# Kernel optimization log

Measured on AMD Instinct MI355X. Metric: run time of the kernel, lower is better.

Reference implementation:

```python
import jax, jax.numpy as jnp
import numpy as np

N = 50000          # total points (25 clouds x 2000 pts)
C = 64             # feature channels (in == out, no bottleneck)
K_NN = 16          # neighbors kept per dilation branch
DILATIONS = (1, 2, 4)
KMAX = K_NN * max(DILATIONS)   # base kNN graph has k*d_max neighbors per node
B = 25             # number of point clouds
EPS = 1e-16


def setup_inputs() -> dict:
    key = jax.random.key(0)
    ks = jax.random.split(key, 8)
    x = jax.random.normal(ks[0], (N, C), jnp.float32)
    pos = jax.random.normal(ks[1], (N, 3), jnp.float32)
    # kNN-style edge_index [2, N*KMAX]: row0 = source/neighbor j, row1 = center i,
    # KMAX consecutive edges per center node, neighbors restricted to the same cloud.
    pts = N // B
    cloud_base = (jnp.arange(N) // pts) * pts
    src = cloud_base[:, None] + jax.random.randint(ks[2], (N, KMAX), 0, pts)
    dst = jnp.broadcast_to(jnp.arange(N)[:, None], (N, KMAX))
    edge_index = jnp.stack([src.reshape(-1), dst.reshape(-1)]).astype(jnp.int32)
    batch = jnp.repeat(jnp.arange(B), pts).astype(jnp.int32)
    nD = len(DILATIONS)
    s = 1.0 / np.sqrt(C)
    Wv = jax.random.normal(ks[3], (nD, C, C), jnp.float32) * s   # lin (value)
    Wq = jax.random.normal(ks[4], (nD, C, C), jnp.float32) * s   # lin_dst
    Wk = jax.random.normal(ks[5], (nD, C, C), jnp.float32) * s   # lin_src
    Wp = jax.random.normal(ks[6], (nD, 3, C), jnp.float32) * (1.0 / np.sqrt(3.0))  # pos_nn
    bp = jax.random.normal(ks[7], (nD, C), jnp.float32) * 0.01
    return dict(x=x, pos=pos, Wv=Wv, Wq=Wq, Wk=Wk, Wp=Wp, bp=bp,
                edge_index=edge_index, batch=batch)


def _dilated_edges(edge_index, k, d):
    # take every d-th of the first k*d neighbors within each node's block -> k edges/node
    e = edge_index.reshape(2, -1, KMAX)[:, :, : k * d : d]
    return e.reshape(2, -1)


def _segment_softmax(a, seg, n):
    amax = jax.ops.segment_max(a, seg, num_segments=n)
    e = jnp.exp(a - amax[seg])
    s = jax.ops.segment_sum(e, seg, num_segments=n)
    return e / (s[seg] + EPS)


def _pt_conv(x, pos, src, dst, Wv, Wq, Wk, Wp, bp):
    # PyG PointTransformerConv: msg = softmax_i(q_i - k_j + delta_ij) * (v_j + delta_ij)
    n = x.shape[0]
    q = x @ Wq        # [N, C]  (lin_dst)
    kk = x @ Wk       # [N, C]  (lin_src)
    v = x @ Wv        # [N, C]  (lin, value)
    delta = (pos[dst] - pos[src]) @ Wp + bp            # [E, C] positional encoding
    alpha = _segment_softmax(q[dst] - kk[src] + delta, dst, n)
    return jax.ops.segment_sum(alpha * (v[src] + delta), dst, num_segments=n)


def reference(x, pos, Wv, Wq, Wk, Wp, bp, edge_index, batch):
    inputs = x
    res = None
    for i, d in enumerate(DILATIONS):
        e = _dilated_edges(edge_index, K_NN, d)
        h = _pt_conv(x, pos, e[0], e[1], Wv[i], Wq[i], Wk[i], Wp[i], bp[i])
        res = h if res is None else jnp.maximum(res, h)   # stack+max over branches
    # global max pool per cloud, gathered back per node
    pool = jax.ops.segment_max(x, batch, num_segments=B)[batch]
    res = jnp.maximum(res, pool)
    return res + inputs   # residual
```

## Files before the change

kernel.cpp:

```cpp
#include <hip/hip_runtime.h>
#include <math.h>

#define NP 50000
#define CH 64
#define KMAX 64
#define KNN 16
#define NB 25
#define PTS (NP / NB)
#define EPSF 1e-16f
#define NTILES (NP / 16)
#define ATILES (NP / 4)
#define L2E 1.4426950408889634f
#define LN2 0.6931471805599453f

typedef __attribute__((ext_vector_type(8))) short short8;
typedef __attribute__((ext_vector_type(4))) float float4v;
typedef __attribute__((ext_vector_type(4))) unsigned int uint4v;
typedef __attribute__((ext_vector_type(2))) unsigned int uint2v;
typedef __attribute__((ext_vector_type(4))) unsigned short ushort4v;

__device__ __forceinline__ ushort f2b(float f) {
  unsigned u = __float_as_uint(f);
  unsigned r = (u + 0x7FFFu + ((u >> 16) & 1u)) >> 16;
  return (ushort)r;
}
__device__ __forceinline__ float b2f(ushort h) {
  return __uint_as_float(((unsigned)h) << 16);
}

#define QBF_BYTES   ((size_t)3 * NP * CH * 2)
#define KVP_BYTES   ((size_t)3 * NP * CH * 4)
#define XBF_BYTES   ((size_t)NP * CH * 2)
#define WPACK_ELEMS (9 * 4 * 2 * 64 * 8)
#define XV (NP * CH / 4)

__global__ __launch_bounds__(256) void prep_kernel(
    const float* __restrict__ x,
    const float* __restrict__ Wv,
    const float* __restrict__ Wq,
    const float* __restrict__ Wk,
    ushort* __restrict__ x_bf,
    ushort* __restrict__ wpack,
    float* __restrict__ pool) {
  const int tid = threadIdx.x;
  const int bid = blockIdx.x;
  __shared__ float red[4][CH];

  if (bid < NB) {
    const int lane = tid & 63;
    const int wave = tid >> 6;
    const float* xb = x + (size_t)bid * PTS * CH;
    float m0 = -INFINITY, m1 = -INFINITY, m2 = -INFINITY, m3 = -INFINITY;
    for (int r = wave * 4; r < PTS; r += 16) {
      m0 = fmaxf(m0, xb[(size_t)(r + 0) * CH + lane]);
      m1 = fmaxf(m1, xb[(size_t)(r + 1) * CH + lane]);
      m2 = fmaxf(m2, xb[(size_t)(r + 2) * CH + lane]);
      m3 = fmaxf(m3, xb[(size_t)(r + 3) * CH + lane]);
    }
    red[wave][lane] = fmaxf(fmaxf(m0, m1), fmaxf(m2, m3));
    __syncthreads();
    if (wave == 0) {
      pool[bid * CH + lane] = fmaxf(fmaxf(red[0][lane], red[1][lane]),
                                    fmaxf(red[2][lane], red[3][lane]));
    }
  } else {
    const int gid = (bid - NB) * 256 + tid;
    if (gid < XV) {
      const float4* xv = (const float4*)x;
      float4 v = xv[gid];
      ushort4v o;
      o[0] = f2b(v.x); o[1] = f2b(v.y); o[2] = f2b(v.z); o[3] = f2b(v.w);
      *(ushort4v*)(x_bf + (size_t)gid * 4) = o;
    } else {
      int pid = gid - XV;
      if (pid < WPACK_ELEMS) {
        int j     = pid & 7;
        int lane  = (pid >> 3) & 63;
        int kstep = (pid >> 9) & 1;
        int mtile = (pid >> 10) & 3;
        int mat   = pid >> 12;
        const float* W;
        int d;
        float scale;
        if (mat < 3)      { W = Wq; d = mat;     scale = L2E; }
        else if (mat < 6) { W = Wk; d = mat - 3; scale = L2E; }
        else              { W = Wv; d = mat - 6; scale = 1.f; }
        int oc = mtile * 16 + (lane & 15);
        int ic = kstep * 32 + ((lane >> 4) & 3) * 8 + j;
        wpack[pid] = f2b(W[d * CH * CH + ic * CH + oc] * scale);
      }
    }
  }
}

__global__ __launch_bounds__(256) void qkv_mfma(
    const ushort* __restrict__ x_bf,
    const ushort* __restrict__ wpack,
    ushort* __restrict__ qbf,
    unsigned int* __restrict__ kvp) {
  const int lane = threadIdx.x;
  const int tile = blockIdx.x * 4 + threadIdx.y;
  if (tile >= NTILES) return;
  const int y = blockIdx.y;
  const int kbase = (lane >> 4) * 8;
  const int myNode = tile * 16 + (lane & 15);
  const ushort* xr = x_bf + (size_t)myNode * CH;
  short8 b0 = *(const short8*)(xr + kbase);
  short8 b1 = *(const short8*)(xr + 32 + kbase);

  if (y < 3) {
    const int dd = y;
    ushort* outQ = qbf + (size_t)dd * NP * CH;
#pragma unroll
    for (int mt = 0; mt < 4; ++mt) {
      short8 a0 = *(const short8*)(wpack +
          ((((size_t)dd * 4 + mt) * 2 + 0) * 64 + lane) * 8);
      short8 a1 = *(const short8*)(wpack +
          ((((size_t)dd * 4 + mt) * 2 + 1) * 64 + lane) * 8);
      float4v acc = {0.f, 0.f, 0.f, 0.f};
      acc = __builtin_amdgcn_mfma_f32_16x16x32_bf16(a0, b0, acc, 0, 0, 0);
      acc = __builtin_amdgcn_mfma_f32_16x16x32_bf16(a1, b1, acc, 0, 0, 0);
      int oc = mt * 16 + (lane >> 4) * 4;
      uint2v o;
      o[0] = (unsigned)f2b(acc[0]) | ((unsigned)f2b(acc[1]) << 16);
      o[1] = (unsigned)f2b(acc[2]) | ((unsigned)f2b(acc[3]) << 16);
      *(uint2v*)(outQ + (size_t)myNode * CH + oc) = o;
    }
  } else {
    const int dd = y - 3;
    unsigned int* outKV = kvp + (size_t)dd * NP * CH;
#pragma unroll
    for (int mt = 0; mt < 4; ++mt) {
      short8 k0 = *(const short8*)(wpack +
          ((((size_t)(3 + dd) * 4 + mt) * 2 + 0) * 64 + lane) * 8);
      short8 k1 = *(const short8*)(wpack +
          ((((size_t)(3 + dd) * 4 + mt) * 2 + 1) * 64 + lane) * 8);
      short8 v0 = *(const short8*)(wpack +
          ((((size_t)(6 + dd) * 4 + mt) * 2 + 0) * 64 + lane) * 8);
      short8 v1 = *(const short8*)(wpack +
          ((((size_t)(6 + dd) * 4 + mt) * 2 + 1) * 64 + lane) * 8);
      float4v aK = {0.f, 0.f, 0.f, 0.f};
      float4v aV = {0.f, 0.f, 0.f, 0.f};
      aK = __builtin_amdgcn_mfma_f32_16x16x32_bf16(k0, b0, aK, 0, 0, 0);
      aK = __builtin_amdgcn_mfma_f32_16x16x32_bf16(k1, b1, aK, 0, 0, 0);
      aV = __builtin_amdgcn_mfma_f32_16x16x32_bf16(v0, b0, aV, 0, 0, 0);
      aV = __builtin_amdgcn_mfma_f32_16x16x32_bf16(v1, b1, aV, 0, 0, 0);
      int oc = mt * 16 + (lane >> 4) * 4;
      uint4v o;
#pragma unroll
      for (int i = 0; i < 4; ++i)
        o[i] = ((unsigned)f2b(aK[i]) << 16) | (unsigned)f2b(aV[i]);
      *(uint4v*)(outKV + (size_t)myNode * CH + oc) = o;
    }
  }
}

__global__ __launch_bounds__(384, 6) void attn_kernel(
    const float* __restrict__ x,
    const float* __restrict__ pos,
    const float* __restrict__ Wp,
    const float* __restrict__ bp,
    const int*   __restrict__ edge_src,
    const ushort* __restrict__ qbf,
    const unsigned int* __restrict__ kvp,
    const float* __restrict__ pool,
    float* __restrict__ out) {
  const int bx  = blockIdx.x;
  const int xcd = bx & 7;
  const int kk  = bx >> 3;
  const int base = (ATILES * xcd) >> 3;
  const int cnt  = ((ATILES * (xcd + 1)) >> 3) - base;
  if (kk >= cnt) return;
  const int node0 = (base + kk) * 4;

  const int wy   = threadIdx.y;
  const int dd   = wy % 3;
  const int half = wy / 3;
  const int tid  = wy * 64 + threadIdx.x;

  __shared__ float sEdge[4 * 260];
  __shared__ float sPartS[3 * 4 * 68];
  __shared__ float sPartA[3 * 4 * 68];
  __shared__ float sRes[2 * 4 * 68];

  if (tid < 256) {
    int nl = tid >> 6, p = tid & 63;
    int nd = node0 + nl;
    int j = edge_src[(size_t)nd * KMAX + p];
    float4v w;
    w[0] = pos[nd * 3 + 0] - pos[j * 3 + 0];
    w[1] = pos[nd * 3 + 1] - pos[j * 3 + 1];
    w[2] = pos[nd * 3 + 2] - pos[j * 3 + 2];
    w[3] = __int_as_float(j << 8);
    *(float4v*)&sEdge[nl * 260 + p * 4] = w;
  }
  __syncthreads();

  const int lane = threadIdx.x;
  const int g    = lane >> 4;
  const int cl   = lane & 15;
  const int node = node0 + g;
  const float* sMy = &sEdge[g * 260];
  const unsigned clOfs = (unsigned)(cl << 4);

  float4v bq, wp0, wp1, wp2;
  {
    ushort4v qh = *(const ushort4v*)(qbf + ((size_t)dd * NP + node) * CH + cl * 4);
    const float* WpD = Wp + dd * 192;
    wp0 = *(const float4v*)(WpD + 0 * 64 + cl * 4) * L2E;
    wp1 = *(const float4v*)(WpD + 1 * 64 + cl * 4) * L2E;
    wp2 = *(const float4v*)(WpD + 2 * 64 + cl * 4) * L2E;
    float4v bpv = *(const float4v*)(bp + dd * 64 + cl * 4);
#pragma unroll
    for (int i = 0; i < 4; ++i) bq[i] = b2f(qh[i]) + bpv[i] * L2E;
  }
  const char* KVb = (const char*)(kvp + (size_t)dd * NP * CH);

  float4v s    = {0.f, 0.f, 0.f, 0.f};
  float4v accv = {0.f, 0.f, 0.f, 0.f};
#pragma unroll
  for (int e = 0; e < 8; ++e) {
    const int p = (half * 8 + e) << dd;
    float4v w = *(const float4v*)(sMy + p * 4);
    uint4v u = *(const uint4v*)(KVb + (__float_as_uint(w[3]) + clOfs));
    float4v kf, vf, wgt;
#pragma unroll
    for (int i = 0; i < 4; ++i) kf[i] = __uint_as_float(u[i] & 0xFFFF0000u);
#pragma unroll
    for (int i = 0; i < 4; ++i) vf[i] = __uint_as_float(u[i] << 16);
    float4v t = bq + w[0] * wp0 + w[1] * wp1 + w[2] * wp2;
    float4v a = t - kf;
#pragma unroll
    for (int i = 0; i < 4; ++i) wgt[i] = __builtin_amdgcn_exp2f(a[i]);
    s += wgt;
    float4v vt;
#pragma unroll
    for (int i = 0; i < 4; ++i) vt[i] = fmaf(LN2, t[i], vf[i]);
    accv += wgt * vt;
  }

  if (half == 1) {
    *(float4v*)&sPartS[(dd * 4 + g) * 68 + cl * 4] = s;
    *(float4v*)&sPartA[(dd * 4 + g) * 68 + cl * 4] = accv;
  }
  __syncthreads();

  float4v r;
  if (half == 0) {
    float4v s2 = *(const float4v*)&sPartS[(dd * 4 + g) * 68 + cl * 4];
    float4v a2 = *(const float4v*)&sPartA[(dd * 4 + g) * 68 + cl * 4];
    s += s2;
    accv += a2;
    float4v bpv = *(const float4v*)(bp + dd * 64 + cl * 4);
#pragma unroll
    for (int i = 0; i < 4; ++i) {
      float q = (bq[i] - bpv[i] * L2E) * LN2;
      r[i] = accv[i] * __builtin_amdgcn_rcpf(s[i] + EPSF) - q;
    }
    if (dd > 0)
      *(float4v*)&sRes[((dd - 1) * 4 + g) * 68 + cl * 4] = r;
  }
  __syncthreads();

  if (wy == 0) {
    float4v r1 = *(const float4v*)&sRes[(0 * 4 + g) * 68 + cl * 4];
    float4v r2 = *(const float4v*)&sRes[(1 * 4 + g) * 68 + cl * 4];
    const int b = node / PTS;
    float4v pv = *(const float4v*)(pool + b * CH + cl * 4);
    float4v xv = *(const float4v*)(x + (size_t)node * CH + cl * 4);
    float4v res;
#pragma unroll
    for (int i = 0; i < 4; ++i)
      res[i] = fmaxf(fmaxf(fmaxf(r[i], r1[i]), r2[i]), pv[i]) + xv[i];
    *(float4v*)(out + (size_t)node * CH + cl * 4) = res;
  }
}

extern "C" void kernel_launch(void* const* d_in, const int* in_sizes, int n_in,
                              void* d_out, int out_size, void* d_ws, size_t ws_size,
                              hipStream_t stream) {
  const float* x    = (const float*)d_in[0];
  const float* pos  = (const float*)d_in[1];
  const float* Wv   = (const float*)d_in[2];
  const float* Wq   = (const float*)d_in[3];
  const float* Wk   = (const float*)d_in[4];
  const float* Wp   = (const float*)d_in[5];
  const float* bp   = (const float*)d_in[6];
  const int*   ei   = (const int*)d_in[7];
  float* out = (float*)d_out;

  char* wsb = (char*)d_ws;
  ushort* qbf   = (ushort*)wsb;
  unsigned int* kvp = (unsigned int*)(wsb + QBF_BYTES);
  ushort* x_bf  = (ushort*)(wsb + QBF_BYTES + KVP_BYTES);
  ushort* wpack = (ushort*)(wsb + QBF_BYTES + KVP_BYTES + XBF_BYTES);
  float*  pool  = (float*)(wsb + QBF_BYTES + KVP_BYTES + XBF_BYTES +
                           (size_t)WPACK_ELEMS * 2);

  {
    int convBlocks = (XV + WPACK_ELEMS + 255) / 256;
    dim3 grid(NB + convBlocks);
    hipLaunchKernelGGL(prep_kernel, grid, dim3(256), 0, stream,
                       x, Wv, Wq, Wk, x_bf, wpack, pool);
  }
  {
    dim3 grid((NTILES + 3) / 4, 6);
    dim3 block(64, 4);
    hipLaunchKernelGGL(qkv_mfma, grid, block, 0, stream, x_bf, wpack, qbf, kvp);
  }
  {
    dim3 grid(8 * ((ATILES + 7) / 8));
    dim3 block(64, 6);
    hipLaunchKernelGGL(attn_kernel, grid, block, 0, stream,
                       x, pos, Wp, bp, ei, qbf, kvp, pool, out);
  }
}
```

Baseline: 218.2 us.

## Split per-cloud max pool across blocks and merge attention halves in one sync

The global max pool now runs over 8 partial blocks per cloud instead of one, so the 25 long-running pool blocks no longer set the tail of the prep kernel. The attention kernel subtracts q*s per half before reduction, so both halves write partial sums and wave 0 does the combine, divide and branch max, removing one __syncthreads and a shared-memory round trip. Consumers now read and reduce 8 partial pool rows per node.

New measurement: 186.7 us. 1.17x faster.

```diff
diff --git a/kernel.cpp b/kernel.cpp
--- a/kernel.cpp
+++ b/kernel.cpp
@@ -12,6 +12,8 @@
 #define ATILES (NP / 4)
 #define L2E 1.4426950408889634f
 #define LN2 0.6931471805599453f
+#define PPB 8
+#define PROWS (PTS / PPB)
 
 typedef __attribute__((ext_vector_type(8))) short short8;
 typedef __attribute__((ext_vector_type(4))) float float4v;
@@ -41,30 +43,30 @@
     const float* __restrict__ Wk,
     ushort* __restrict__ x_bf,
     ushort* __restrict__ wpack,
-    float* __restrict__ pool) {
+    float* __restrict__ poolP) {
   const int tid = threadIdx.x;
   const int bid = blockIdx.x;
   __shared__ float red[4][CH];
 
-  if (bid < NB) {
+  if (bid < NB * PPB) {
     const int lane = tid & 63;
     const int wave = tid >> 6;
-    const float* xb = x + (size_t)bid * PTS * CH;
-    float m0 = -INFINITY, m1 = -INFINITY, m2 = -INFINITY, m3 = -INFINITY;
-    for (int r = wave * 4; r < PTS; r += 16) {
+    const int cloud = bid >> 3;
+    const int part  = bid & 7;
+    const float* xb = x + ((size_t)cloud * PTS + part * PROWS) * CH;
+    float m0 = -INFINITY, m1 = -INFINITY;
+    for (int r = wave * 2; r < PROWS; r += 8) {
       m0 = fmaxf(m0, xb[(size_t)(r + 0) * CH + lane]);
       m1 = fmaxf(m1, xb[(size_t)(r + 1) * CH + lane]);
-      m2 = fmaxf(m2, xb[(size_t)(r + 2) * CH + lane]);
-      m3 = fmaxf(m3, xb[(size_t)(r + 3) * CH + lane]);
-    }
-    red[wave][lane] = fmaxf(fmaxf(m0, m1), fmaxf(m2, m3));
+    }
+    red[wave][lane] = fmaxf(m0, m1);
     __syncthreads();
     if (wave == 0) {
-      pool[bid * CH + lane] = fmaxf(fmaxf(red[0][lane], red[1][lane]),
-                                    fmaxf(red[2][lane], red[3][lane]));
+      poolP[(size_t)bid * CH + lane] = fmaxf(fmaxf(red[0][lane], red[1][lane]),
+                                             fmaxf(red[2][lane], red[3][lane]));
     }
   } else {
-    const int gid = (bid - NB) * 256 + tid;
+    const int gid = (bid - NB * PPB) * 256 + tid;
     if (gid < XV) {
       const float4* xv = (const float4*)x;
       float4 v = xv[gid];
@@ -163,7 +165,7 @@
     const int*   __restrict__ edge_src,
     const ushort* __restrict__ qbf,
     const unsigned int* __restrict__ kvp,
-    const float* __restrict__ pool,
+    const float* __restrict__ poolP,
     float* __restrict__ out) {
   const int bx  = blockIdx.x;
   const int xcd = bx & 7;
@@ -179,9 +181,8 @@
   const int tid  = wy * 64 + threadIdx.x;
 
   __shared__ float sEdge[4 * 260];
-  __shared__ float sPartS[3 * 4 * 68];
-  __shared__ float sPartA[3 * 4 * 68];
-  __shared__ float sRes[2 * 4 * 68];
+  __shared__ float sS[6 * 4 * 68];
+  __shared__ float sP[6 * 4 * 68];
 
   if (tid < 256) {
     int nl = tid >> 6, p = tid & 63;
@@ -200,10 +201,9 @@
   const int g    = lane >> 4;
   const int cl   = lane & 15;
   const int node = node0 + g;
-  const float* sMy = &sEdge[g * 260];
   const unsigned clOfs = (unsigned)(cl << 4);
 
-  float4v bq, wp0, wp1, wp2;
+  float4v bq, qorig, wp0, wp1, wp2;
   {
     ushort4v qh = *(const ushort4v*)(qbf + ((size_t)dd * NP + node) * CH + cl * 4);
     const float* WpD = Wp + dd * 192;
@@ -211,17 +211,23 @@
     wp1 = *(const float4v*)(WpD + 1 * 64 + cl * 4) * L2E;
     wp2 = *(const float4v*)(WpD + 2 * 64 + cl * 4) * L2E;
     float4v bpv = *(const float4v*)(bp + dd * 64 + cl * 4);
-#pragma unroll
-    for (int i = 0; i < 4; ++i) bq[i] = b2f(qh[i]) + bpv[i] * L2E;
+    float4v qf;
+#pragma unroll
+    for (int i = 0; i < 4; ++i) qf[i] = b2f(qh[i]);
+    bq = qf + bpv * L2E;
+    qorig = qf * LN2;
   }
   const char* KVb = (const char*)(kvp + (size_t)dd * NP * CH);
+
+  const float* ep = &sEdge[g * 260] + (((half * 8) << dd) * 4);
+  const int estep = (1 << dd) * 4;
 
   float4v s    = {0.f, 0.f, 0.f, 0.f};
   float4v accv = {0.f, 0.f, 0.f, 0.f};
 #pragma unroll
   for (int e = 0; e < 8; ++e) {
-    const int p = (half * 8 + e) << dd;
-    float4v w = *(const float4v*)(sMy + p * 4);
+    float4v w = *(const float4v*)ep;
+    ep += estep;
     uint4v u = *(const uint4v*)(KVb + (__float_as_uint(w[3]) + clOfs));
     float4v kf, vf, wgt;
 #pragma unroll
@@ -233,45 +239,46 @@
 #pragma unroll
     for (int i = 0; i < 4; ++i) wgt[i] = __builtin_amdgcn_exp2f(a[i]);
     s += wgt;
-    float4v vt;
-#pragma unroll
-    for (int i = 0; i < 4; ++i) vt[i] = fmaf(LN2, t[i], vf[i]);
-    accv += wgt * vt;
-  }
-
-  if (half == 1) {
-    *(float4v*)&sPartS[(dd * 4 + g) * 68 + cl * 4] = s;
-    *(float4v*)&sPartA[(dd * 4 + g) * 68 + cl * 4] = accv;
-  }
+    accv += wgt * (vf + t * LN2);
+  }
+
+  float4v P = accv - qorig * s;
+  *(float4v*)&sS[(wy * 4 + g) * 68 + cl * 4] = s;
+  *(float4v*)&sP[(wy * 4 + g) * 68 + cl * 4] = P;
   __syncthreads();
 
-  float4v r;
-  if (half == 0) {
-    float4v s2 = *(const float4v*)&sPartS[(dd * 4 + g) * 68 + cl * 4];
-    float4v a2 = *(const float4v*)&sPartA[(dd * 4 + g) * 68 + cl * 4];
-    s += s2;
-    accv += a2;
-    float4v bpv = *(const float4v*)(bp + dd * 64 + cl * 4);
-#pragma unroll
-    for (int i = 0; i < 4; ++i) {
-      float q = (bq[i] - bpv[i] * L2E) * LN2;
-      r[i] = accv[i] * __builtin_amdgcn_rcpf(s[i] + EPSF) - q;
-    }
-    if (dd > 0)
-      *(float4v*)&sRes[((dd - 1) * 4 + g) * 68 + cl * 4] = r;
-  }
-  __syncthreads();
-
   if (wy == 0) {
-    float4v r1 = *(const float4v*)&sRes[(0 * 4 + g) * 68 + cl * 4];
-    float4v r2 = *(const float4v*)&sRes[(1 * 4 + g) * 68 + cl * 4];
+    float4v res;
+#pragma unroll
+    for (int d2 = 0; d2 < 3; ++d2) {
+      float4v s0 = *(const float4v*)&sS[((d2    ) * 4 + g) * 68 + cl * 4];
+      float4v s1 = *(const float4v*)&sS[((d2 + 3) * 4 + g) * 68 + cl * 4];
+      float4v p0 = *(const float4v*)&sP[((d2    ) * 4 + g) * 68 + cl * 4];
+      float4v p1 = *(const float4v*)&sP[((d2 + 3) * 4 + g) * 68 + cl * 4];
+      float4v st = s0 + s1;
+      float4v pt = p0 + p1;
+      float4v r;
+#pragma unroll
+      for (int i = 0; i < 4; ++i)
+        r[i] = pt[i] * __builtin_amdgcn_rcpf(st[i] + EPSF);
+      if (d2 == 0) res = r;
+      else {
+#pragma unroll
+        for (int i = 0; i < 4; ++i) res[i] = fmaxf(res[i], r[i]);
+      }
+    }
     const int b = node / PTS;
-    float4v pv = *(const float4v*)(pool + b * CH + cl * 4);
+    const float* pp = poolP + (size_t)(b * PPB) * CH + cl * 4;
+    float4v pv = *(const float4v*)pp;
+#pragma unroll
+    for (int q2 = 1; q2 < PPB; ++q2) {
+      float4v t2 = *(const float4v*)(pp + (size_t)q2 * CH);
+#pragma unroll
+      for (int i = 0; i < 4; ++i) pv[i] = fmaxf(pv[i], t2[i]);
+    }
     float4v xv = *(const float4v*)(x + (size_t)node * CH + cl * 4);
-    float4v res;
-#pragma unroll
-    for (int i = 0; i < 4; ++i)
-      res[i] = fmaxf(fmaxf(fmaxf(r[i], r1[i]), r2[i]), pv[i]) + xv[i];
+#pragma unroll
+    for (int i = 0; i < 4; ++i) res[i] = fmaxf(res[i], pv[i]) + xv[i];
     *(float4v*)(out + (size_t)node * CH + cl * 4) = res;
   }
 }
@@ -294,14 +301,14 @@
   unsigned int* kvp = (unsigned int*)(wsb + QBF_BYTES);
   ushort* x_bf  = (ushort*)(wsb + QBF_BYTES + KVP_BYTES);
   ushort* wpack = (ushort*)(wsb + QBF_BYTES + KVP_BYTES + XBF_BYTES);
-  float*  pool  = (float*)(wsb + QBF_BYTES + KVP_BYTES + XBF_BYTES +
+  float*  poolP = (float*)(wsb + QBF_BYTES + KVP_BYTES + XBF_BYTES +
                            (size_t)WPACK_ELEMS * 2);
 
   {
     int convBlocks = (XV + WPACK_ELEMS + 255) / 256;
-    dim3 grid(NB + convBlocks);
+    dim3 grid(NB * PPB + convBlocks);
     hipLaunchKernelGGL(prep_kernel, grid, dim3(256), 0, stream,
-                       x, Wv, Wq, Wk, x_bf, wpack, pool);
+                       x, Wv, Wq, Wk, x_bf, wpack, poolP);
   }
   {
     dim3 grid((NTILES + 3) / 4, 6);
@@ -312,6 +319,6 @@
     dim3 grid(8 * ((ATILES + 7) / 8));
     dim3 block(64, 6);
     hipLaunchKernelGGL(attn_kernel, grid, block, 0, stream,
-                       x, pos, Wp, bp, ei, qbf, kvp, pool, out);
-  }
-}
+                       x, pos, Wp, bp, ei, qbf, kvp, poolP, out);
+  }
+}
```
